# Performance work log

Measured on AMD Instinct MI355X. Metric: run time of the kernel, lower is better.

Reference implementation:

```python
import jax, jax.numpy as jnp
import numpy as np

N = 100000   # nodes
E = 1200000  # edges (avg degree 12)
D = 64       # feature dim (in == hidden == out, forced by residual add)
L = 3        # num_layers


def setup_inputs() -> dict:
    key = jax.random.key(0)
    ks = jax.random.split(key, 8)
    s = 1.0 / np.float32(np.sqrt(D))
    x = jax.random.normal(ks[0], (N, D), jnp.float32)
    edge_index = jax.random.randint(ks[1], (2, E), 0, N, dtype=jnp.int32)
    W1 = jax.random.normal(ks[2], (L, D, D), jnp.float32) * s
    b1 = jnp.zeros((L, D), jnp.float32)
    W2 = jax.random.normal(ks[3], (L, D, D), jnp.float32) * s
    b2 = jnp.zeros((L, D), jnp.float32)
    Wf = jax.random.normal(ks[4], (D, D), jnp.float32) * s
    bf = jnp.zeros((D,), jnp.float32)
    return {"x": x, "edge_index": edge_index, "W1": W1, "b1": b1,
            "W2": W2, "b2": b2, "Wf": Wf, "bf": bf}


def reference(x, edge_index, W1, b1, W2, b2, Wf, bf):
    row, col = edge_index[0], edge_index[1]
    h = x
    for l in range(L):
        def mlp(z):
            # Linear -> ReLU -> Linear (same MLP applied to messages and combine)
            return jnp.maximum(z @ W1[l] + b1[l], 0.0) @ W2[l] + b2[l]
        msgs = mlp(h[col])                                        # [E, D] gather + MLP
        agg = jax.ops.segment_sum(msgs, row, num_segments=N)      # [N, D] scatter-add
        h = mlp(h + agg)                                          # residual combine + MLP
    return h @ Wf + bf
```

## Files before the change

### kernel.cpp

```cpp
#include <hip/hip_runtime.h>

typedef unsigned int uint;
typedef unsigned short ushort;
typedef __attribute__((ext_vector_type(8))) short short8;
typedef __attribute__((ext_vector_type(4))) float f32x4;
typedef __attribute__((ext_vector_type(4))) int i32x4;

#define DIM 64
#define MAXDEG 48
#define NBUCKET 8

__device__ __forceinline__ ushort f2bf(float f) {
    uint u = __float_as_uint(f);
    u += 0x7fffu + ((u >> 16) & 1u);
    return (ushort)(u >> 16);
}
__device__ __forceinline__ float bf2f(ushort h) {
    return __uint_as_float(((uint)h) << 16);
}

__global__ __launch_bounds__(256) void f32_to_bf16(
    const float4* __restrict__ in, ushort4* __restrict__ out, int n4)
{
    int i = blockIdx.x * blockDim.x + threadIdx.x;
    if (i >= n4) return;
    float4 v = in[i];
    ushort4 o;
    o.x = f2bf(v.x); o.y = f2bf(v.y); o.z = f2bf(v.z); o.w = f2bf(v.w);
    out[i] = o;
}

__global__ __launch_bounds__(256, 4) void mlp_mfma(
    const ushort* __restrict__ in, ushort* __restrict__ out,
    const float* __restrict__ W1, const float* __restrict__ b1,
    const float* __restrict__ W2, const float* __restrict__ b2,
    int ntiles)
{
    __shared__ __align__(16) ushort lds[4][16 * 72];
    const int lane = threadIdx.x & 63;
    const int wid  = threadIdx.x >> 6;
    const int c = lane & 15, g = lane >> 4;
    ushort* myl = &lds[wid][0];

    short8 wf[2][2][4];
#pragma unroll
    for (int kc = 0; kc < 2; ++kc)
#pragma unroll
        for (int t = 0; t < 4; ++t)
#pragma unroll
            for (int j = 0; j < 8; ++j) {
                wf[0][kc][t][j] = (short)f2bf(W1[(kc * 32 + g * 8 + j) * 64 + t * 16 + c]);
                wf[1][kc][t][j] = (short)f2bf(W2[(kc * 32 + g * 8 + j) * 64 + t * 16 + c]);
            }
    float bc1[4], bc2[4];
#pragma unroll
    for (int t = 0; t < 4; ++t) { bc1[t] = b1[t * 16 + c]; bc2[t] = b2[t * 16 + c]; }

    const int gw = (int)((blockIdx.x * blockDim.x + threadIdx.x) >> 6);
    const int nw = (int)((gridDim.x * blockDim.x) >> 6);

    for (int tile = gw; tile < ntiles; tile += nw) {
        const ushort* rp = in + (size_t)(tile * 16 + c) * DIM;
        short8 a0 = *(const short8*)(rp + g * 8);
        short8 a1 = *(const short8*)(rp + 32 + g * 8);

        f32x4 acc[4];
#pragma unroll
        for (int t = 0; t < 4; ++t) {
            f32x4 z = {0.f, 0.f, 0.f, 0.f};
            z = __builtin_amdgcn_mfma_f32_16x16x32_bf16(a0, wf[0][0][t], z, 0, 0, 0);
            z = __builtin_amdgcn_mfma_f32_16x16x32_bf16(a1, wf[0][1][t], z, 0, 0, 0);
            acc[t] = z;
        }
#pragma unroll
        for (int t = 0; t < 4; ++t)
#pragma unroll
            for (int r = 0; r < 4; ++r) {
                float v = fmaxf(acc[t][r] + bc1[t], 0.f);
                myl[(4 * g + r) * 72 + 16 * t + c] = f2bf(v);
            }
        short8 h0 = *(const short8*)(myl + c * 72 + g * 8);
        short8 h1 = *(const short8*)(myl + c * 72 + 32 + g * 8);

#pragma unroll
        for (int t = 0; t < 4; ++t) {
            f32x4 z = {0.f, 0.f, 0.f, 0.f};
            z = __builtin_amdgcn_mfma_f32_16x16x32_bf16(h0, wf[1][0][t], z, 0, 0, 0);
            z = __builtin_amdgcn_mfma_f32_16x16x32_bf16(h1, wf[1][1][t], z, 0, 0, 0);
#pragma unroll
            for (int r = 0; r < 4; ++r)
                myl[(4 * g + r) * 72 + 16 * t + c] = f2bf(z[r] + bc2[t]);
        }
        const ushort* lp = myl + (lane >> 2) * 72 + (lane & 3) * 8;
        short8 ov0 = *(const short8*)lp;
        short8 ov1 = *(const short8*)(lp + 32);
        ushort* op = out + (size_t)(tile * 16 + (lane >> 2)) * DIM + (lane & 3) * 8;
        *(short8*)op = ov0;
        *(short8*)(op + 32) = ov1;
    }
}

__global__ __launch_bounds__(256) void linear_mfma(
    const ushort* __restrict__ in, float* __restrict__ out,
    const float* __restrict__ Wg, const float* __restrict__ bg, int ntiles)
{
    const int lane = threadIdx.x & 63;
    const int c = lane & 15, g = lane >> 4;

    short8 wf[2][2][4];
#pragma unroll
    for (int kc = 0; kc < 2; ++kc)
#pragma unroll
        for (int t = 0; t < 4; ++t)
#pragma unroll
            for (int j = 0; j < 8; ++j) {
                float wv = Wg[(kc * 32 + g * 8 + j) * 64 + t * 16 + c];
                ushort h = f2bf(wv); ushort l = f2bf(wv - bf2f(h));
                wf[0][kc][t][j] = (short)h; wf[1][kc][t][j] = (short)l;
            }
    float bc[4];
#pragma unroll
    for (int t = 0; t < 4; ++t) bc[t] = bg[t * 16 + c];

    const int gw = (int)((blockIdx.x * blockDim.x + threadIdx.x) >> 6);
    const int nw = (int)((gridDim.x * blockDim.x) >> 6);

    for (int tile = gw; tile < ntiles; tile += nw) {
        const ushort* rp = in + (size_t)(tile * 16 + c) * DIM;
        short8 a0 = *(const short8*)(rp + g * 8);
        short8 a1 = *(const short8*)(rp + 32 + g * 8);
#pragma unroll
        for (int t = 0; t < 4; ++t) {
            f32x4 z = {0.f, 0.f, 0.f, 0.f};
            z = __builtin_amdgcn_mfma_f32_16x16x32_bf16(a0, wf[0][0][t], z, 0, 0, 0);
            z = __builtin_amdgcn_mfma_f32_16x16x32_bf16(a1, wf[0][1][t], z, 0, 0, 0);
            z = __builtin_amdgcn_mfma_f32_16x16x32_bf16(a0, wf[1][0][t], z, 0, 0, 0);
            z = __builtin_amdgcn_mfma_f32_16x16x32_bf16(a1, wf[1][1][t], z, 0, 0, 0);
#pragma unroll
            for (int r = 0; r < 4; ++r)
                out[(size_t)(tile * 16 + 4 * g + r) * DIM + 16 * t + c] = z[r] + bc[t];
        }
    }
}

__global__ __launch_bounds__(256) void fill_ell_bucketed(
    const int* __restrict__ rowi, const int* __restrict__ coli,
    int* __restrict__ cnt, int* __restrict__ ell, int E, int nper)
{
    const int bucket = blockIdx.x & (NBUCKET - 1);
    const int bpb = gridDim.x / NBUCKET;
    const int bidx = blockIdx.x >> 3;
    const int lo = bucket * nper;
    const int hi = lo + nper;
    const int stride = bpb * 256;
    const int e4n = E >> 2;

    for (int i = bidx * 256 + threadIdx.x; i < e4n; i += stride) {
        i32x4 r4 = __builtin_nontemporal_load((const i32x4*)rowi + i);
        i32x4 c4 = __builtin_nontemporal_load((const i32x4*)coli + i);
#pragma unroll
        for (int u = 0; u < 4; ++u) {
            int r = r4[u];
            if (r >= lo && r < hi) {
                int slot = atomicAdd(&cnt[r], 1);
                if (slot < MAXDEG) ell[(size_t)r * MAXDEG + slot] = c4[u];
            }
        }
    }
}

__global__ __launch_bounds__(256) void gather_kernel(
    const ushort* __restrict__ m, const ushort* __restrict__ h,
    const int* __restrict__ ell, const int* __restrict__ cnt,
    ushort* __restrict__ t, int N)
{
    const int lane = threadIdx.x & 63;
    const int node = (int)((blockIdx.x * blockDim.x + threadIdx.x) >> 6);
    if (node >= N) return;
    int deg = cnt[node];
    deg = deg < MAXDEG ? deg : MAXDEG;
    const int* el = ell + (size_t)node * MAXDEG;

    float a0 = bf2f(h[(size_t)node * DIM + lane]);
    float a1 = 0.f, a2 = 0.f, a3 = 0.f, a4 = 0.f, a5 = 0.f, a6 = 0.f, a7 = 0.f;
    int i = 0;
    for (; i + 8 <= deg; i += 8) {
        int4 q0 = *(const int4*)(el + i);
        int4 q1 = *(const int4*)(el + i + 4);
        a0 += bf2f(m[(size_t)q0.x * DIM + lane]);
        a1 += bf2f(m[(size_t)q0.y * DIM + lane]);
        a2 += bf2f(m[(size_t)q0.z * DIM + lane]);
        a3 += bf2f(m[(size_t)q0.w * DIM + lane]);
        a4 += bf2f(m[(size_t)q1.x * DIM + lane]);
        a5 += bf2f(m[(size_t)q1.y * DIM + lane]);
        a6 += bf2f(m[(size_t)q1.z * DIM + lane]);
        a7 += bf2f(m[(size_t)q1.w * DIM + lane]);
    }
    if (i + 4 <= deg) {
        int4 q = *(const int4*)(el + i);
        a0 += bf2f(m[(size_t)q.x * DIM + lane]);
        a1 += bf2f(m[(size_t)q.y * DIM + lane]);
        a2 += bf2f(m[(size_t)q.z * DIM + lane]);
        a3 += bf2f(m[(size_t)q.w * DIM + lane]);
        i += 4;
    }
    for (; i < deg; ++i)
        a0 += bf2f(m[(size_t)el[i] * DIM + lane]);
    t[(size_t)node * DIM + lane] =
        f2bf(((a0 + a1) + (a2 + a3)) + ((a4 + a5) + (a6 + a7)));
}

extern "C" void kernel_launch(void* const* d_in, const int* in_sizes, int n_in,
                              void* d_out, int out_size, void* d_ws, size_t ws_size,
                              hipStream_t stream)
{
    const float* x  = (const float*)d_in[0];
    const int*   ei = (const int*)d_in[1];
    const float* W1 = (const float*)d_in[2];
    const float* b1 = (const float*)d_in[3];
    const float* W2 = (const float*)d_in[4];
    const float* b2 = (const float*)d_in[5];
    const float* Wf = (const float*)d_in[6];
    const float* bf = (const float*)d_in[7];
    float* out = (float*)d_out;

    const int N = in_sizes[0] / DIM;
    const int E = in_sizes[1] / 2;
    const int NT = N / 16;

    ushort* hA = (ushort*)d_ws;
    ushort* hB = hA + (size_t)N * DIM;
    ushort* hC = hB + (size_t)N * DIM;
    int* cnt = (int*)(hC + (size_t)N * DIM);
    int* ell = cnt + N;

    f32_to_bf16<<<(N * DIM / 4 + 255) / 256, 256, 0, stream>>>(
        (const float4*)x, (ushort4*)hA, N * DIM / 4);
    (void)hipMemsetAsync(cnt, 0, (size_t)N * sizeof(int), stream);
    fill_ell_bucketed<<<4096, 256, 0, stream>>>(
        ei, ei + E, cnt, ell, E, (N + NBUCKET - 1) / NBUCKET);

    for (int l = 0; l < 3; ++l) {
        const float* w1  = W1 + (size_t)l * DIM * DIM;
        const float* w2  = W2 + (size_t)l * DIM * DIM;
        const float* bb1 = b1 + (size_t)l * DIM;
        const float* bb2 = b2 + (size_t)l * DIM;
        mlp_mfma<<<1024, 256, 0, stream>>>(hA, hB, w1, bb1, w2, bb2, NT);
        gather_kernel<<<(N * 64 + 255) / 256, 256, 0, stream>>>(hB, hA, ell, cnt, hC, N);
        mlp_mfma<<<1024, 256, 0, stream>>>(hC, hA, w1, bb1, w2, bb2, NT);
    }
    linear_mfma<<<1024, 256, 0, stream>>>(hA, out, Wf, bf, NT);
}
```

Measured before the change: 354.3 us.

## Pre-pack bf16 weight fragments and gather 8 nodes per wave with 16B loads

A small kernel now converts W1/W2/Wf once into a per-lane packed bf16 fragment layout. The MLP and final linear kernels then load their MFMA weight fragments with vector loads, replacing the strided fp32 loads and conversions each block did before. The gather kernel now assigns 8 lanes per node, each reading 8 bf16 values with one 16-byte load, instead of one lane per feature with 2-byte loads. This trades a smaller unroll (4 neighbours per step) and more per-lane accumulators for fewer, wider memory transactions.

```diff
diff --git a/kernel.cpp b/kernel.cpp
--- a/kernel.cpp
+++ b/kernel.cpp
@@ -30,10 +30,42 @@
     out[i] = o;
 }
 
+__global__ void pack_weights(
+    const float* __restrict__ W1, const float* __restrict__ W2,
+    const float* __restrict__ Wf, ushort* __restrict__ wp, ushort* __restrict__ lp)
+{
+    const int lane = threadIdx.x;
+    const int c = lane & 15, g = lane >> 4;
+    if (blockIdx.x < 3) {
+        const int l = blockIdx.x;
+        const float* w1 = W1 + (size_t)l * 4096;
+        const float* w2 = W2 + (size_t)l * 4096;
+        ushort* d0 = wp + ((size_t)(l * 2 + 0) * 64 + lane) * 64;
+        ushort* d1 = wp + ((size_t)(l * 2 + 1) * 64 + lane) * 64;
+        for (int kc = 0; kc < 2; ++kc)
+            for (int t = 0; t < 4; ++t)
+                for (int j = 0; j < 8; ++j) {
+                    int src = (kc * 32 + g * 8 + j) * 64 + t * 16 + c;
+                    d0[(kc * 4 + t) * 8 + j] = f2bf(w1[src]);
+                    d1[(kc * 4 + t) * 8 + j] = f2bf(w2[src]);
+                }
+    } else {
+        for (int kc = 0; kc < 2; ++kc)
+            for (int t = 0; t < 4; ++t)
+                for (int j = 0; j < 8; ++j) {
+                    float wv = Wf[(kc * 32 + g * 8 + j) * 64 + t * 16 + c];
+                    ushort h = f2bf(wv);
+                    ushort l = f2bf(wv - bf2f(h));
+                    lp[(size_t)lane * 128 + ((0 * 2 + kc) * 4 + t) * 8 + j] = h;
+                    lp[(size_t)lane * 128 + ((1 * 2 + kc) * 4 + t) * 8 + j] = l;
+                }
+    }
+}
+
 __global__ __launch_bounds__(256, 4) void mlp_mfma(
     const ushort* __restrict__ in, ushort* __restrict__ out,
-    const float* __restrict__ W1, const float* __restrict__ b1,
-    const float* __restrict__ W2, const float* __restrict__ b2,
+    const ushort* __restrict__ wp,
+    const float* __restrict__ b1, const float* __restrict__ b2,
     int ntiles)
 {
     __shared__ __align__(16) ushort lds[4][16 * 72];
@@ -42,16 +74,16 @@
     const int c = lane & 15, g = lane >> 4;
     ushort* myl = &lds[wid][0];
 
+    const ushort* w0 = wp + (size_t)lane * 64;
+    const ushort* w1p = wp + (size_t)(64 + lane) * 64;
     short8 wf[2][2][4];
 #pragma unroll
     for (int kc = 0; kc < 2; ++kc)
 #pragma unroll
-        for (int t = 0; t < 4; ++t)
-#pragma unroll
-            for (int j = 0; j < 8; ++j) {
-                wf[0][kc][t][j] = (short)f2bf(W1[(kc * 32 + g * 8 + j) * 64 + t * 16 + c]);
-                wf[1][kc][t][j] = (short)f2bf(W2[(kc * 32 + g * 8 + j) * 64 + t * 16 + c]);
-            }
+        for (int t = 0; t < 4; ++t) {
+            wf[0][kc][t] = *(const short8*)(w0 + (kc * 4 + t) * 8);
+            wf[1][kc][t] = *(const short8*)(w1p + (kc * 4 + t) * 8);
+        }
     float bc1[4], bc2[4];
 #pragma unroll
     for (int t = 0; t < 4; ++t) { bc1[t] = b1[t * 16 + c]; bc2[t] = b2[t * 16 + c]; }
@@ -91,9 +123,9 @@
             for (int r = 0; r < 4; ++r)
                 myl[(4 * g + r) * 72 + 16 * t + c] = f2bf(z[r] + bc2[t]);
         }
-        const ushort* lp = myl + (lane >> 2) * 72 + (lane & 3) * 8;
-        short8 ov0 = *(const short8*)lp;
-        short8 ov1 = *(const short8*)(lp + 32);
+        const ushort* lp2 = myl + (lane >> 2) * 72 + (lane & 3) * 8;
+        short8 ov0 = *(const short8*)lp2;
+        short8 ov1 = *(const short8*)(lp2 + 32);
         ushort* op = out + (size_t)(tile * 16 + (lane >> 2)) * DIM + (lane & 3) * 8;
         *(short8*)op = ov0;
         *(short8*)(op + 32) = ov1;
@@ -102,22 +134,19 @@
 
 __global__ __launch_bounds__(256) void linear_mfma(
     const ushort* __restrict__ in, float* __restrict__ out,
-    const float* __restrict__ Wg, const float* __restrict__ bg, int ntiles)
+    const ushort* __restrict__ lpw, const float* __restrict__ bg, int ntiles)
 {
     const int lane = threadIdx.x & 63;
     const int c = lane & 15, g = lane >> 4;
 
     short8 wf[2][2][4];
 #pragma unroll
-    for (int kc = 0; kc < 2; ++kc)
-#pragma unroll
-        for (int t = 0; t < 4; ++t)
-#pragma unroll
-            for (int j = 0; j < 8; ++j) {
-                float wv = Wg[(kc * 32 + g * 8 + j) * 64 + t * 16 + c];
-                ushort h = f2bf(wv); ushort l = f2bf(wv - bf2f(h));
-                wf[0][kc][t][j] = (short)h; wf[1][kc][t][j] = (short)l;
-            }
+    for (int s = 0; s < 2; ++s)
+#pragma unroll
+        for (int kc = 0; kc < 2; ++kc)
+#pragma unroll
+            for (int t = 0; t < 4; ++t)
+                wf[s][kc][t] = *(const short8*)(lpw + (size_t)lane * 128 + ((s * 2 + kc) * 4 + t) * 8);
     float bc[4];
 #pragma unroll
     for (int t = 0; t < 4; ++t) bc[t] = bg[t * 16 + c];
@@ -169,45 +198,47 @@
     }
 }
 
-__global__ __launch_bounds__(256) void gather_kernel(
+__global__ __launch_bounds__(256) void gather8_kernel(
     const ushort* __restrict__ m, const ushort* __restrict__ h,
     const int* __restrict__ ell, const int* __restrict__ cnt,
     ushort* __restrict__ t, int N)
 {
     const int lane = threadIdx.x & 63;
-    const int node = (int)((blockIdx.x * blockDim.x + threadIdx.x) >> 6);
+    const int wave = (int)((blockIdx.x * blockDim.x + threadIdx.x) >> 6);
+    const int sub = lane >> 3, chunk = lane & 7;
+    const int node = wave * 8 + sub;
     if (node >= N) return;
     int deg = cnt[node];
     deg = deg < MAXDEG ? deg : MAXDEG;
     const int* el = ell + (size_t)node * MAXDEG;
-
-    float a0 = bf2f(h[(size_t)node * DIM + lane]);
-    float a1 = 0.f, a2 = 0.f, a3 = 0.f, a4 = 0.f, a5 = 0.f, a6 = 0.f, a7 = 0.f;
+    const int roff = chunk * 8;
+
+    float acc[8];
+    short8 hv = *(const short8*)(h + (size_t)node * DIM + roff);
+#pragma unroll
+    for (int j = 0; j < 8; ++j) acc[j] = bf2f((ushort)hv[j]);
+
     int i = 0;
-    for (; i + 8 <= deg; i += 8) {
-        int4 q0 = *(const int4*)(el + i);
-        int4 q1 = *(const int4*)(el + i + 4);
-        a0 += bf2f(m[(size_t)q0.x * DIM + lane]);
-        a1 += bf2f(m[(size_t)q0.y * DIM + lane]);
-        a2 += bf2f(m[(size_t)q0.z * DIM + lane]);
-        a3 += bf2f(m[(size_t)q0.w * DIM + lane]);
-        a4 += bf2f(m[(size_t)q1.x * DIM + lane]);
-        a5 += bf2f(m[(size_t)q1.y * DIM + lane]);
-        a6 += bf2f(m[(size_t)q1.z * DIM + lane]);
-        a7 += bf2f(m[(size_t)q1.w * DIM + lane]);
-    }
-    if (i + 4 <= deg) {
+    for (; i + 4 <= deg; i += 4) {
         int4 q = *(const int4*)(el + i);
-        a0 += bf2f(m[(size_t)q.x * DIM + lane]);
-        a1 += bf2f(m[(size_t)q.y * DIM + lane]);
-        a2 += bf2f(m[(size_t)q.z * DIM + lane]);
-        a3 += bf2f(m[(size_t)q.w * DIM + lane]);
-        i += 4;
-    }
-    for (; i < deg; ++i)
-        a0 += bf2f(m[(size_t)el[i] * DIM + lane]);
-    t[(size_t)node * DIM + lane] =
-        f2bf(((a0 + a1) + (a2 + a3)) + ((a4 + a5) + (a6 + a7)));
+        short8 r0 = *(const short8*)(m + (size_t)q.x * DIM + roff);
+        short8 r1 = *(const short8*)(m + (size_t)q.y * DIM + roff);
+        short8 r2 = *(const short8*)(m + (size_t)q.z * DIM + roff);
+        short8 r3 = *(const short8*)(m + (size_t)q.w * DIM + roff);
+#pragma unroll
+        for (int j = 0; j < 8; ++j)
+            acc[j] += (bf2f((ushort)r0[j]) + bf2f((ushort)r1[j]))
+                    + (bf2f((ushort)r2[j]) + bf2f((ushort)r3[j]));
+    }
+    for (; i < deg; ++i) {
+        short8 r = *(const short8*)(m + (size_t)el[i] * DIM + roff);
+#pragma unroll
+        for (int j = 0; j < 8; ++j) acc[j] += bf2f((ushort)r[j]);
+    }
+    short8 o;
+#pragma unroll
+    for (int j = 0; j < 8; ++j) o[j] = (short)f2bf(acc[j]);
+    *(short8*)(t + (size_t)node * DIM + roff) = o;
 }
 
 extern "C" void kernel_launch(void* const* d_in, const int* in_sizes, int n_in,
@@ -233,21 +264,24 @@
     ushort* hC = hB + (size_t)N * DIM;
     int* cnt = (int*)(hC + (size_t)N * DIM);
     int* ell = cnt + N;
+    ushort* wpack = (ushort*)(ell + (size_t)N * MAXDEG);
+    ushort* lpack = wpack + 6 * 64 * 64;
 
     f32_to_bf16<<<(N * DIM / 4 + 255) / 256, 256, 0, stream>>>(
         (const float4*)x, (ushort4*)hA, N * DIM / 4);
     (void)hipMemsetAsync(cnt, 0, (size_t)N * sizeof(int), stream);
     fill_ell_bucketed<<<4096, 256, 0, stream>>>(
         ei, ei + E, cnt, ell, E, (N + NBUCKET - 1) / NBUCKET);
+    pack_weights<<<4, 64, 0, stream>>>(W1, W2, Wf, wpack, lpack);
 
     for (int l = 0; l < 3; ++l) {
-        const float* w1  = W1 + (size_t)l * DIM * DIM;
-        const float* w2  = W2 + (size_t)l * DIM * DIM;
+        const ushort* wp = wpack + (size_t)l * 2 * 64 * 64;
         const float* bb1 = b1 + (size_t)l * DIM;
         const float* bb2 = b2 + (size_t)l * DIM;
-        mlp_mfma<<<1024, 256, 0, stream>>>(hA, hB, w1, bb1, w2, bb2, NT);
-        gather_kernel<<<(N * 64 + 255) / 256, 256, 0, stream>>>(hB, hA, ell, cnt, hC, N);
-        mlp_mfma<<<1024, 256, 0, stream>>>(hC, hA, w1, bb1, w2, bb2, NT);
-    }
-    linear_mfma<<<1024, 256, 0, stream>>>(hA, out, Wf, bf, NT);
-}
+        mlp_mfma<<<1024, 256, 0, stream>>>(hA, hB, wp, bb1, bb2, NT);
+        gather8_kernel<<<(N / 8 * 64 + 255) / 256, 256, 0, stream>>>(
+            hB, hA, ell, cnt, hC, N);
+        mlp_mfma<<<1024, 256, 0, stream>>>(hC, hA, wp, bb1, bb2, NT);
+    }
+    linear_mfma<<<1024, 256, 0, stream>>>(hA, out, lpack, bf, NT);
+}
```

Result: faster. 339.2 us (-4.2%).
